# Kernel tuning notes

Hardware: AMD Instinct MI355X
Metric: run time of the kernel (lower is better)

## Reference

```python
import jax, jax.numpy as jnp
import numpy as np

RADIUS = 1.3
N_SAMPLES = 256
STEP = 0.0176


def trilinear(grid, pts):
    """grid: [C, D, H, W]; pts: [M, 3] in [-1, 1] ordered (x, y, z) like torch grid_sample
    (x indexes W, y indexes H, z indexes D), align_corners=True, border padding.
    Returns [M, C]."""
    C, D, H, W = grid.shape
    sizes = jnp.asarray([W, H, D], dtype=pts.dtype)
    co = jnp.clip((pts + 1.0) * 0.5 * (sizes - 1.0), 0.0, sizes - 1.0)
    c0 = jnp.floor(co)
    f = co - c0                                   # [M,3] trilinear weights
    i0 = c0.astype(jnp.int32)
    i1 = jnp.minimum(i0 + 1, jnp.asarray([W - 1, H - 1, D - 1], jnp.int32))
    gf = grid.reshape(C, -1)

    def gat(ix, iy, iz):                          # -> [M, C]
        return gf[:, (iz * H + iy) * W + ix].T

    x0, y0, z0 = i0[:, 0], i0[:, 1], i0[:, 2]
    x1, y1, z1 = i1[:, 0], i1[:, 1], i1[:, 2]
    wx, wy, wz = f[:, 0:1], f[:, 1:2], f[:, 2:3]
    out = (gat(x0, y0, z0) * (1 - wx) * (1 - wy) * (1 - wz)
         + gat(x1, y0, z0) * wx       * (1 - wy) * (1 - wz)
         + gat(x0, y1, z0) * (1 - wx) * wy       * (1 - wz)
         + gat(x1, y1, z0) * wx       * wy       * (1 - wz)
         + gat(x0, y0, z1) * (1 - wx) * (1 - wy) * wz
         + gat(x1, y0, z1) * wx       * (1 - wy) * wz
         + gat(x0, y1, z1) * (1 - wx) * wy       * wz
         + gat(x1, y1, z1) * wx       * wy       * wz)
    return out


def get_intersections(rays_o, dirn):
    """Ray / cube[-R,R]^3 intersection; N_SAMPLES uniform steps from entry point.
    Returns pts [B,N,3], t-values [B,N], validity mask [B,N]."""
    eps = 1e-9
    safe_d = jnp.where(jnp.abs(dirn) < eps, eps, dirn)
    inv = 1.0 / safe_d
    t1 = (-RADIUS - rays_o) * inv
    t2 = (RADIUS - rays_o) * inv
    tmin = jnp.max(jnp.minimum(t1, t2), axis=-1)
    tmax = jnp.min(jnp.maximum(t1, t2), axis=-1)
    tnear = jnp.maximum(tmin, 0.0)
    hit = tmax > tnear                                          # [B]
    t = tnear[:, None] + STEP * jnp.arange(N_SAMPLES, dtype=rays_o.dtype)[None, :]
    pts = rays_o[:, None, :] + t[..., None] * dirn[:, None, :]  # [B,N,3]
    mask = (t < tmax[:, None]) & hit[:, None]
    return pts, t, mask


def setup_inputs() -> dict:
    key = jax.random.key(0)
    ks = jax.random.split(key, 12)
    B, R, GD, FD, NF, HW = 2048, 128, 3, 32, 32, 64
    o = jax.random.normal(ks[0], (B, 3), dtype=jnp.float32)
    rays_o = o / jnp.linalg.norm(o, axis=-1, keepdims=True) * (2.0 * RADIUS)
    rays_d = -rays_o + 0.3 * jax.random.normal(ks[1], (B, 3), dtype=jnp.float32)
    G1 = 0.01 * jax.random.normal(ks[2], (GD, R, R, R), dtype=jnp.float32)
    F = 0.05 * jax.random.normal(ks[3], (FD, NF, NF, NF), dtype=jnp.float32)
    s = 0.1
    return {
        'rays_o': rays_o, 'rays_d': rays_d, 'G1': G1, 'F': F,
        'Wd1': s * jax.random.normal(ks[4], (FD, HW), dtype=jnp.float32),
        'bd1': jnp.zeros((HW,), jnp.float32),
        'Wd2': s * jax.random.normal(ks[5], (HW, 1), dtype=jnp.float32),
        'bd2': jnp.zeros((1,), jnp.float32),
        'Wc1': s * jax.random.normal(ks[6], (FD + 3, HW), dtype=jnp.float32),
        'bc1': jnp.zeros((HW,), jnp.float32),
        'Wc2': s * jax.random.normal(ks[7], (HW, 3), dtype=jnp.float32),
        'bc2': jnp.zeros((3,), jnp.float32),
    }


def reference(rays_o, rays_d, G1, F, Wd1, bd1, Wd2, bd2, Wc1, bc1, Wc2, bc2):
    B = rays_o.shape[0]
    dirn = rays_d / jnp.linalg.norm(rays_d, axis=-1, keepdims=True)
    pts, t, mask = get_intersections(rays_o, dirn)           # [B,N,3],[B,N],[B,N]
    pts_n = (pts / RADIUS).reshape(-1, 3)                     # [M,3] in ~[-1,1]

    # nested multi-grid trilinear lookups: coords -> G1 -> F
    g1v = trilinear(G1, pts_n)                                # [M,3]
    feats = trilinear(F, g1v)                                 # [M,feature_dim]

    # density MLP (1 hidden layer, width 64)
    h = jax.nn.relu(feats @ Wd1 + bd1)
    sigma = (h @ Wd2 + bd2)[:, 0].reshape(B, N_SAMPLES)
    sigma = jnp.where(mask, sigma, 0.0)

    # sigma -> alpha -> compositing weights (abs_light)
    dists = jnp.concatenate([t[:, 1:] - t[:, :-1],
                             jnp.full((B, 1), STEP, t.dtype)], axis=1)
    alpha = 1.0 - jnp.exp(-jax.nn.relu(sigma) * dists)
    T = jnp.cumprod(1.0 - alpha + 1e-10, axis=1)
    T_excl = jnp.concatenate([jnp.ones((B, 1), alpha.dtype), T[:, :-1]], axis=1)
    weights = alpha * T_excl                                  # [B,N]

    # color MLP conditioned on view direction
    dflat = jnp.broadcast_to(dirn[:, None, :], (B, N_SAMPLES, 3)).reshape(-1, 3)
    hc = jax.nn.relu(jnp.concatenate([feats, dflat], axis=-1) @ Wc1 + bc1)
    rgb = jax.nn.sigmoid((hc @ Wc2 + bc2).reshape(B, N_SAMPLES, 3))
    rgb = jnp.where(mask[..., None], rgb, 0.0)

    out = jnp.sum(weights[..., None] * rgb, axis=1)           # [B,3]
    acc = jnp.sum(weights, axis=1)
    return out + (1.0 - acc)[:, None]                         # white background
```

## Files before the change

### kernel.cpp

```cpp
#include <hip/hip_runtime.h>
#include <hip/hip_fp16.h>
#include <math.h>

#define NSAMP 256

typedef _Float16 f16;
typedef _Float16 f16x8 __attribute__((ext_vector_type(8)));
typedef float    f32x4 __attribute__((ext_vector_type(4)));

__global__ __launch_bounds__(256) void transpose_F(
    const float* __restrict__ Fg, float* __restrict__ Ft)
{
    const int j = blockIdx.x * 256 + threadIdx.x;
    float4 o[8];
    #pragma unroll
    for (int q = 0; q < 8; ++q) {
        o[q].x = Fg[(size_t)(4*q+0)*32768 + j];
        o[q].y = Fg[(size_t)(4*q+1)*32768 + j];
        o[q].z = Fg[(size_t)(4*q+2)*32768 + j];
        o[q].w = Fg[(size_t)(4*q+3)*32768 + j];
    }
    float4* dst = (float4*)(Ft + (size_t)j * 32);
    #pragma unroll
    for (int q = 0; q < 8; ++q) dst[q] = o[q];
}

__global__ __launch_bounds__(256) void pack_bfrags(
    const float* __restrict__ Wd1, const float* __restrict__ Wc1,
    f16* __restrict__ Bd, f16* __restrict__ Bc)
{
    const int idx  = threadIdx.x;
    const int nt   = idx >> 6;
    const int lane = idx & 63;
    const int j    = nt*16 + (lane & 15);
    const int k0   = (lane >> 4) * 8;
    f16x8 vd, vc;
    #pragma unroll
    for (int i = 0; i < 8; ++i) {
        vd[i] = (f16)Wd1[(k0+i)*64 + j];
        vc[i] = (f16)Wc1[(k0+i)*64 + j];
    }
    *(f16x8*)(Bd + ((size_t)(nt*64+lane))*8) = vd;
    *(f16x8*)(Bc + ((size_t)(nt*64+lane))*8) = vc;
}

template<bool USE_MFMA>
__global__ __launch_bounds__(256) __attribute__((amdgpu_waves_per_eu(2, 6)))
void nerf_fused(
    const float* __restrict__ rays_o, const float* __restrict__ rays_d,
    const float* __restrict__ G1, const float* __restrict__ Fg,
    const float* __restrict__ Wd1, const float* __restrict__ bd1,
    const float* __restrict__ Wd2, const float* __restrict__ bd2,
    const float* __restrict__ Wc1, const float* __restrict__ bc1,
    const float* __restrict__ Wc2, const float* __restrict__ bc2,
    const float* __restrict__ Ft,
    const f16* __restrict__ Bd, const f16* __restrict__ Bc,
    float* __restrict__ out)
{
    const float RADIUS = 1.3f;
    const float STEP = 0.0176f;

    const int b    = blockIdx.x;
    const int tid  = threadIdx.x;
    const int lane = tid & 63;
    const int wv   = tid >> 6;

    __shared__ __align__(16) f16 feats_lds[256][32];
    __shared__ float sig_lds[256];
    __shared__ f16   rgb_lds[256][4];
    __shared__ float s_wtot[4];
    __shared__ float s_red[4][4];

    const float ox = rays_o[b*3+0], oy = rays_o[b*3+1], oz = rays_o[b*3+2];
    const float rdx = rays_d[b*3+0], rdy = rays_d[b*3+1], rdz = rays_d[b*3+2];
    const float rn  = sqrtf(rdx*rdx + rdy*rdy + rdz*rdz);
    const float dxn = rdx/rn, dyn = rdy/rn, dzn = rdz/rn;

    float sd, inv, t1, t2, tmin, tmax;
    sd = (fabsf(dxn) < 1e-9f) ? 1e-9f : dxn; inv = 1.0f/sd;
    t1 = (-RADIUS - ox)*inv; t2 = (RADIUS - ox)*inv;
    tmin = fminf(t1,t2); tmax = fmaxf(t1,t2);
    sd = (fabsf(dyn) < 1e-9f) ? 1e-9f : dyn; inv = 1.0f/sd;
    t1 = (-RADIUS - oy)*inv; t2 = (RADIUS - oy)*inv;
    tmin = fmaxf(tmin, fminf(t1,t2)); tmax = fminf(tmax, fmaxf(t1,t2));
    sd = (fabsf(dzn) < 1e-9f) ? 1e-9f : dzn; inv = 1.0f/sd;
    t1 = (-RADIUS - oz)*inv; t2 = (RADIUS - oz)*inv;
    tmin = fmaxf(tmin, fminf(t1,t2)); tmax = fminf(tmax, fmaxf(t1,t2));

    const float tnear = fmaxf(tmin, 0.0f);
    const bool  hit   = tmax > tnear;
    const float t     = tnear + STEP * (float)tid;
    const bool  mask  = (t < tmax) && hit;

    const bool wave_active = __any(mask);

    float sigma = 0.0f, rr = 0.0f, rg = 0.0f, rb = 0.0f;

    float feats[32];
    if (wave_active) {
        const float invR = 1.0f / RADIUS;
        const float px = (ox + t*dxn) * invR;
        const float py = (oy + t*dyn) * invR;
        const float pz = (oz + t*dzn) * invR;

        float cox = fminf(fmaxf((px+1.0f)*0.5f*127.0f, 0.0f), 127.0f);
        float coy = fminf(fmaxf((py+1.0f)*0.5f*127.0f, 0.0f), 127.0f);
        float coz = fminf(fmaxf((pz+1.0f)*0.5f*127.0f, 0.0f), 127.0f);
        int x0 = (int)floorf(cox); float fx = cox - (float)x0; int x1 = min(x0+1, 127);
        int y0 = (int)floorf(coy); float fy = coy - (float)y0; int y1 = min(y0+1, 127);
        int z0 = (int)floorf(coz); float fz = coz - (float)z0; int z1 = min(z0+1, 127);

        {
            const float wx0 = 1.0f-fx, wx1 = fx;
            const float wy0 = 1.0f-fy, wy1 = fy;
            const float wz0 = 1.0f-fz, wz1 = fz;
            const float w000 = wx0*wy0*wz0, w100 = wx1*wy0*wz0;
            const float w010 = wx0*wy1*wz0, w110 = wx1*wy1*wz0;
            const float w001 = wx0*wy0*wz1, w101 = wx1*wy0*wz1;
            const float w011 = wx0*wy1*wz1, w111 = wx1*wy1*wz1;
            const int i000 = (z0*128 + y0)*128 + x0;
            const int dxo = x1 - x0;
            const int dyo = (y1 - y0)*128;
            const int dzo = (z1 - z0)*16384;
            const int i100 = i000 + dxo,       i010 = i000 + dyo;
            const int i110 = i000 + dyo + dxo, i001 = i000 + dzo;
            const int i101 = i000 + dzo + dxo, i011 = i000 + dzo + dyo;
            const int i111 = i000 + dzo + dyo + dxo;

            float g[3];
            #pragma unroll
            for (int c = 0; c < 3; ++c) {
                const float* gp = G1 + (size_t)c * 2097152;
                g[c] = w000*gp[i000] + w100*gp[i100] + w010*gp[i010] + w110*gp[i110]
                     + w001*gp[i001] + w101*gp[i101] + w011*gp[i011] + w111*gp[i111];
            }

            cox = fminf(fmaxf((g[0]+1.0f)*0.5f*31.0f, 0.0f), 31.0f);
            coy = fminf(fmaxf((g[1]+1.0f)*0.5f*31.0f, 0.0f), 31.0f);
            coz = fminf(fmaxf((g[2]+1.0f)*0.5f*31.0f, 0.0f), 31.0f);
            x0 = (int)floorf(cox); fx = cox - (float)x0; x1 = min(x0+1, 31);
            y0 = (int)floorf(coy); fy = coy - (float)y0; y1 = min(y0+1, 31);
            z0 = (int)floorf(coz); fz = coz - (float)z0; z1 = min(z0+1, 31);
        }

        #pragma unroll
        for (int c = 0; c < 32; ++c) feats[c] = 0.0f;
        {
            const float wx0 = 1.0f-fx, wx1 = fx;
            const float wy0 = 1.0f-fy, wy1 = fy;
            const float wz0 = 1.0f-fz, wz1 = fz;
            const int j000 = (z0*32 + y0)*32 + x0;
            const int dxo = x1 - x0;
            const int dyo = (y1 - y0)*32;
            const int dzo = (z1 - z0)*1024;

            const int   jidx[8] = { j000,           j000+dxo,
                                    j000+dyo,       j000+dyo+dxo,
                                    j000+dzo,       j000+dzo+dxo,
                                    j000+dzo+dyo,   j000+dzo+dyo+dxo };
            const float jwt[8]  = { wx0*wy0*wz0, wx1*wy0*wz0,
                                    wx0*wy1*wz0, wx1*wy1*wz0,
                                    wx0*wy0*wz1, wx1*wy0*wz1,
                                    wx0*wy1*wz1, wx1*wy1*wz1 };

            if (USE_MFMA) {
                #pragma unroll
                for (int corner = 0; corner < 8; ++corner) {
                    const float4* fp = (const float4*)(Ft + (size_t)jidx[corner] * 32);
                    const float w = jwt[corner];
                    #pragma unroll
                    for (int q = 0; q < 8; ++q) {
                        const float4 v = fp[q];
                        feats[4*q+0] += w * v.x;
                        feats[4*q+1] += w * v.y;
                        feats[4*q+2] += w * v.z;
                        feats[4*q+3] += w * v.w;
                    }
                }
            } else {
                #pragma unroll
                for (int corner = 0; corner < 8; ++corner) {
                    const float w = jwt[corner];
                    const int  j  = jidx[corner];
                    #pragma unroll
                    for (int c = 0; c < 32; ++c)
                        feats[c] += w * Fg[(size_t)c * 32768 + j];
                }
            }
        }
    }

    if (USE_MFMA) {
        if (wave_active) {
            #pragma unroll
            for (int gq = 0; gq < 4; ++gq) {
                f16x8 h;
                #pragma unroll
                for (int i = 0; i < 8; ++i) h[i] = (f16)feats[gq*8+i];
                *(f16x8*)&feats_lds[tid][gq*8] = h;
            }
        }
        __syncthreads();

        if (wave_active) {
            const int lane15 = lane & 15;
            const int laneg  = lane >> 4;

            float bias_d[4], bias_c[4], wd2v[4];
            float wc2r[4], wc2g[4], wc2b[4];
            #pragma unroll
            for (int nt = 0; nt < 4; ++nt) {
                const int j = nt*16 + lane15;
                bias_d[nt] = bd1[j];
                bias_c[nt] = bc1[j] + dxn*Wc1[32*64+j] + dyn*Wc1[33*64+j] + dzn*Wc1[34*64+j];
                wd2v[nt]   = Wd2[j];
                wc2r[nt]   = Wc2[j*3+0];
                wc2g[nt]   = Wc2[j*3+1];
                wc2b[nt]   = Wc2[j*3+2];
            }
            f16x8 bdf[4], bcf[4];
            #pragma unroll
            for (int nt = 0; nt < 4; ++nt) {
                bdf[nt] = *(const f16x8*)(Bd + ((size_t)(nt*64+lane))*8);
                bcf[nt] = *(const f16x8*)(Bc + ((size_t)(nt*64+lane))*8);
            }

            #pragma unroll
            for (int mt = 0; mt < 4; ++mt) {
                const int arow = wv*64 + mt*16 + lane15;
                const f16x8 af = *(const f16x8*)&feats_lds[arow][laneg*8];

                f32x4 accd[4], accc[4];
                #pragma unroll
                for (int nt = 0; nt < 4; ++nt) {
                    const float bdv = bias_d[nt], bcv = bias_c[nt];
                    accd[nt] = (f32x4){bdv, bdv, bdv, bdv};
                    accc[nt] = (f32x4){bcv, bcv, bcv, bcv};
                }
                #pragma unroll
                for (int nt = 0; nt < 4; ++nt) {
                    accd[nt] = __builtin_amdgcn_mfma_f32_16x16x32_f16(af, bdf[nt], accd[nt], 0, 0, 0);
                    accc[nt] = __builtin_amdgcn_mfma_f32_16x16x32_f16(af, bcf[nt], accc[nt], 0, 0, 0);
                }

                float ss[4] = {0.f,0.f,0.f,0.f};
                float sr[4] = {0.f,0.f,0.f,0.f};
                float sg[4] = {0.f,0.f,0.f,0.f};
                float sb[4] = {0.f,0.f,0.f,0.f};
                #pragma unroll
                for (int nt = 0; nt < 4; ++nt) {
                    #pragma unroll
                    for (int reg = 0; reg < 4; ++reg) {
                        const float hd = fmaxf(accd[nt][reg], 0.0f);
                        ss[reg] += hd * wd2v[nt];
                        const float hc = fmaxf(accc[nt][reg], 0.0f);
                        sr[reg] += hc * wc2r[nt];
                        sg[reg] += hc * wc2g[nt];
                        sb[reg] += hc * wc2b[nt];
                    }
                }
                #pragma unroll
                for (int st = 1; st < 16; st <<= 1) {
                    #pragma unroll
                    for (int reg = 0; reg < 4; ++reg) {
                        ss[reg] += __shfl_xor(ss[reg], st, 64);
                        sr[reg] += __shfl_xor(sr[reg], st, 64);
                        sg[reg] += __shfl_xor(sg[reg], st, 64);
                        sb[reg] += __shfl_xor(sb[reg], st, 64);
                    }
                }
                if (lane15 == 0) {
                    const int base = wv*64 + mt*16 + laneg*4;
                    #pragma unroll
                    for (int reg = 0; reg < 4; ++reg) {
                        sig_lds[base+reg]    = ss[reg];
                        rgb_lds[base+reg][0] = (f16)sr[reg];
                        rgb_lds[base+reg][1] = (f16)sg[reg];
                        rgb_lds[base+reg][2] = (f16)sb[reg];
                    }
                }
            }
        }
        __syncthreads();

        {
            const float sv  = sig_lds[tid];
            const float crv = (float)rgb_lds[tid][0] + bc2[0];
            const float cgv = (float)rgb_lds[tid][1] + bc2[1];
            const float cbv = (float)rgb_lds[tid][2] + bc2[2];
            sigma = mask ? (sv + bd2[0]) : 0.0f;
            rr = mask ? 1.0f/(1.0f + expf(-crv)) : 0.0f;
            rg = mask ? 1.0f/(1.0f + expf(-cgv)) : 0.0f;
            rb = mask ? 1.0f/(1.0f + expf(-cbv)) : 0.0f;
        }
    } else {
        if (wave_active) {
            float sg1 = bd2[0], cr = 0.0f, cg = 0.0f, cb = 0.0f;
            for (int j0 = 0; j0 < 64; j0 += 8) {
                float ad[8], ac[8];
                #pragma unroll
                for (int jj = 0; jj < 8; ++jj) {
                    ad[jj] = bd1[j0+jj];
                    ac[jj] = bc1[j0+jj] + dxn*Wc1[32*64 + j0 + jj]
                                        + dyn*Wc1[33*64 + j0 + jj]
                                        + dzn*Wc1[34*64 + j0 + jj];
                }
                #pragma unroll
                for (int k = 0; k < 32; ++k) {
                    const float fv = feats[k];
                    #pragma unroll
                    for (int jj = 0; jj < 8; ++jj) {
                        ad[jj] += fv * Wd1[k*64 + j0 + jj];
                        ac[jj] += fv * Wc1[k*64 + j0 + jj];
                    }
                }
                #pragma unroll
                for (int jj = 0; jj < 8; ++jj) {
                    sg1 += fmaxf(ad[jj], 0.0f) * Wd2[j0+jj];
                    const float hc = fmaxf(ac[jj], 0.0f);
                    cr += hc * Wc2[(j0+jj)*3 + 0];
                    cg += hc * Wc2[(j0+jj)*3 + 1];
                    cb += hc * Wc2[(j0+jj)*3 + 2];
                }
            }
            cr += bc2[0]; cg += bc2[1]; cb += bc2[2];
            sigma = mask ? sg1 : 0.0f;
            rr = mask ? 1.0f/(1.0f + expf(-cr)) : 0.0f;
            rg = mask ? 1.0f/(1.0f + expf(-cg)) : 0.0f;
            rb = mask ? 1.0f/(1.0f + expf(-cb)) : 0.0f;
        }
    }

    const float alpha = 1.0f - expf(-fmaxf(sigma, 0.0f) * STEP);
    float p = 1.0f - alpha + 1e-10f;

    float scan = p;
    #pragma unroll
    for (int off = 1; off < 64; off <<= 1) {
        const float n = __shfl_up(scan, off, 64);
        if (lane >= off) scan *= n;
    }
    if (lane == 63) s_wtot[wv] = scan;
    __syncthreads();

    float pre = 1.0f;
    #pragma unroll
    for (int q = 0; q < 4; ++q) if (q < wv) pre *= s_wtot[q];
    float excl = __shfl_up(scan, 1, 64);
    if (lane == 0) excl = 1.0f;
    const float Texcl = pre * excl;

    const float w = alpha * Texcl;
    float sw  = w;
    float swr = w * rr, swg = w * rg, swb = w * rb;

    #pragma unroll
    for (int off = 32; off > 0; off >>= 1) {
        sw  += __shfl_down(sw,  off, 64);
        swr += __shfl_down(swr, off, 64);
        swg += __shfl_down(swg, off, 64);
        swb += __shfl_down(swb, off, 64);
    }
    if (lane == 0) {
        s_red[wv][0] = sw;  s_red[wv][1] = swr;
        s_red[wv][2] = swg; s_red[wv][3] = swb;
    }
    __syncthreads();
    if (tid == 0) {
        float W = 0.0f, R = 0.0f, Gc = 0.0f, Bc2_ = 0.0f;
        #pragma unroll
        for (int q = 0; q < 4; ++q) {
            W  += s_red[q][0]; R  += s_red[q][1];
            Gc += s_red[q][2]; Bc2_ += s_red[q][3];
        }
        const float bg = 1.0f - W;
        out[b*3+0] = R  + bg;
        out[b*3+1] = Gc + bg;
        out[b*3+2] = Bc2_ + bg;
    }
}

extern "C" void kernel_launch(void* const* d_in, const int* in_sizes, int n_in,
                              void* d_out, int out_size, void* d_ws, size_t ws_size,
                              hipStream_t stream) {
    const float* rays_o = (const float*)d_in[0];
    const float* rays_d = (const float*)d_in[1];
    const float* G1     = (const float*)d_in[2];
    const float* Fg     = (const float*)d_in[3];
    const float* Wd1    = (const float*)d_in[4];
    const float* bd1    = (const float*)d_in[5];
    const float* Wd2    = (const float*)d_in[6];
    const float* bd2    = (const float*)d_in[7];
    const float* Wc1    = (const float*)d_in[8];
    const float* bc1    = (const float*)d_in[9];
    const float* Wc2    = (const float*)d_in[10];
    const float* bc2    = (const float*)d_in[11];
    float* out = (float*)d_out;

    const int B = in_sizes[0] / 3;
    const size_t ft_bytes = (size_t)32768 * 32 * sizeof(float);
    const size_t bf_bytes = (size_t)4 * 64 * 8 * sizeof(f16);

    if (ws_size >= ft_bytes + 2*bf_bytes) {
        float* Ft = (float*)d_ws;
        f16*   Bd = (f16*)((char*)d_ws + ft_bytes);
        f16*   Bc = (f16*)((char*)d_ws + ft_bytes + bf_bytes);
        transpose_F<<<dim3(128), dim3(256), 0, stream>>>(Fg, Ft);
        pack_bfrags<<<dim3(1), dim3(256), 0, stream>>>(Wd1, Wc1, Bd, Bc);
        nerf_fused<true><<<dim3(B), dim3(NSAMP), 0, stream>>>(
            rays_o, rays_d, G1, Fg, Wd1, bd1, Wd2, bd2, Wc1, bc1, Wc2, bc2,
            Ft, Bd, Bc, out);
    } else {
        nerf_fused<false><<<dim3(B), dim3(NSAMP), 0, stream>>>(
            rays_o, rays_d, G1, Fg, Wd1, bd1, Wd2, bd2, Wc1, bc1, Wc2, bc2,
            Fg, (const f16*)d_ws, (const f16*)d_ws, out);
    }
}
```

Before: 144.9 us.

## Repack grids to fp16 with x-neighbour pairing to halve trilinear gathers

Adds a per-call pre-pass that repacks the 128^3 coordinate grid G1 into fp16 records. Each 16-byte record holds a voxel's 3 channels plus those of its x+1 neighbour. The feature table is also transposed to fp16, with a zero padding row so adjacent rows serve as the x+1 corner. Each trilinear lookup then needs 4 wide loads instead of 8 per corner set, which is meant to cut scattered gather traffic and instruction count. In exchange, every call reads and writes tens of MB of repacked G1 data, and the first-level grid values lose precision in fp16, which feeds into the second-level coordinates.

```diff
diff --git a/kernel.cpp b/kernel.cpp
--- a/kernel.cpp
+++ b/kernel.cpp
@@ -5,24 +5,46 @@
 #define NSAMP 256
 
 typedef _Float16 f16;
+typedef _Float16 f16x4 __attribute__((ext_vector_type(4)));
 typedef _Float16 f16x8 __attribute__((ext_vector_type(8)));
 typedef float    f32x4 __attribute__((ext_vector_type(4)));
 
-__global__ __launch_bounds__(256) void transpose_F(
-    const float* __restrict__ Fg, float* __restrict__ Ft)
+__global__ __launch_bounds__(256) void transpose_F16(
+    const float* __restrict__ Fg, f16* __restrict__ Ft)
 {
     const int j = blockIdx.x * 256 + threadIdx.x;
-    float4 o[8];
-    #pragma unroll
-    for (int q = 0; q < 8; ++q) {
-        o[q].x = Fg[(size_t)(4*q+0)*32768 + j];
-        o[q].y = Fg[(size_t)(4*q+1)*32768 + j];
-        o[q].z = Fg[(size_t)(4*q+2)*32768 + j];
-        o[q].w = Fg[(size_t)(4*q+3)*32768 + j];
-    }
-    float4* dst = (float4*)(Ft + (size_t)j * 32);
-    #pragma unroll
-    for (int q = 0; q < 8; ++q) dst[q] = o[q];
+    f16x8 o[4];
+    #pragma unroll
+    for (int q = 0; q < 4; ++q)
+        #pragma unroll
+        for (int i = 0; i < 8; ++i)
+            o[q][i] = (f16)Fg[(size_t)(8*q+i)*32768 + j];
+    f16* dst = Ft + (size_t)j * 32;
+    #pragma unroll
+    for (int q = 0; q < 4; ++q) *(f16x8*)(dst + q*8) = o[q];
+    if (j == 32767) {
+        f16x8 z = {};
+        f16* pd = Ft + (size_t)32768 * 32;
+        #pragma unroll
+        for (int q = 0; q < 4; ++q) *(f16x8*)(pd + q*8) = z;
+    }
+}
+
+__global__ __launch_bounds__(256) void transpose_G1p(
+    const float* __restrict__ G1, f16x8* __restrict__ G1p)
+{
+    const int v  = blockIdx.x * 256 + threadIdx.x;
+    const int vn = min(v + 1, 2097151);
+    f16x8 o;
+    o[0] = (f16)G1[v];
+    o[1] = (f16)G1[2097152 + v];
+    o[2] = (f16)G1[2*2097152 + v];
+    o[3] = (f16)0.0f;
+    o[4] = (f16)G1[vn];
+    o[5] = (f16)G1[2097152 + vn];
+    o[6] = (f16)G1[2*2097152 + vn];
+    o[7] = (f16)0.0f;
+    G1p[v] = o;
 }
 
 __global__ __launch_bounds__(256) void pack_bfrags(
@@ -44,16 +66,14 @@
     *(f16x8*)(Bc + ((size_t)(nt*64+lane))*8) = vc;
 }
 
-template<bool USE_MFMA>
 __global__ __launch_bounds__(256) __attribute__((amdgpu_waves_per_eu(2, 6)))
-void nerf_fused(
+void nerf_fused_opt(
     const float* __restrict__ rays_o, const float* __restrict__ rays_d,
-    const float* __restrict__ G1, const float* __restrict__ Fg,
-    const float* __restrict__ Wd1, const float* __restrict__ bd1,
-    const float* __restrict__ Wd2, const float* __restrict__ bd2,
+    const f16x8* __restrict__ G1p, const f16* __restrict__ Ft16,
+    const float* __restrict__ bd1, const float* __restrict__ Wd2,
+    const float* __restrict__ bd2,
     const float* __restrict__ Wc1, const float* __restrict__ bc1,
     const float* __restrict__ Wc2, const float* __restrict__ bc2,
-    const float* __restrict__ Ft,
     const f16* __restrict__ Bd, const f16* __restrict__ Bc,
     float* __restrict__ out)
 {
@@ -65,7 +85,7 @@
     const int lane = tid & 63;
     const int wv   = tid >> 6;
 
-    __shared__ __align__(16) f16 feats_lds[256][32];
+    __shared__ __align__(16) f16 feats_lds[256][40];
     __shared__ float sig_lds[256];
     __shared__ f16   rgb_lds[256][4];
     __shared__ float s_wtot[4];
@@ -106,10 +126,283 @@
         float cox = fminf(fmaxf((px+1.0f)*0.5f*127.0f, 0.0f), 127.0f);
         float coy = fminf(fmaxf((py+1.0f)*0.5f*127.0f, 0.0f), 127.0f);
         float coz = fminf(fmaxf((pz+1.0f)*0.5f*127.0f, 0.0f), 127.0f);
+        int x0 = (int)floorf(cox); float fx = cox - (float)x0;
+        int y0 = (int)floorf(coy); float fy = coy - (float)y0; int y1 = min(y0+1, 127);
+        int z0 = (int)floorf(coz); float fz = coz - (float)z0; int z1 = min(z0+1, 127);
+
+        {
+            const float wx0 = 1.0f-fx, wx1 = fx;
+            const float wy0 = 1.0f-fy, wy1 = fy;
+            const float wz0 = 1.0f-fz, wz1 = fz;
+            const int i000 = (z0*128 + y0)*128 + x0;
+            const int dyo = (y1 - y0)*128;
+            const int dzo = (z1 - z0)*16384;
+
+            const f16x8 p00 = G1p[i000];
+            const f16x8 p10 = G1p[i000 + dyo];
+            const f16x8 p01 = G1p[i000 + dzo];
+            const f16x8 p11 = G1p[i000 + dyo + dzo];
+
+            const float a00 = wy0*wz0, a10 = wy1*wz0, a01 = wy0*wz1, a11 = wy1*wz1;
+
+            float g[3];
+            #pragma unroll
+            for (int c = 0; c < 3; ++c) {
+                g[c] = a00*(wx0*(float)p00[c] + wx1*(float)p00[4+c])
+                     + a10*(wx0*(float)p10[c] + wx1*(float)p10[4+c])
+                     + a01*(wx0*(float)p01[c] + wx1*(float)p01[4+c])
+                     + a11*(wx0*(float)p11[c] + wx1*(float)p11[4+c]);
+            }
+
+            cox = fminf(fmaxf((g[0]+1.0f)*0.5f*31.0f, 0.0f), 31.0f);
+            coy = fminf(fmaxf((g[1]+1.0f)*0.5f*31.0f, 0.0f), 31.0f);
+            coz = fminf(fmaxf((g[2]+1.0f)*0.5f*31.0f, 0.0f), 31.0f);
+            x0 = (int)floorf(cox); fx = cox - (float)x0;
+            y0 = (int)floorf(coy); fy = coy - (float)y0; y1 = min(y0+1, 31);
+            z0 = (int)floorf(coz); fz = coz - (float)z0; z1 = min(z0+1, 31);
+        }
+
+        #pragma unroll
+        for (int c = 0; c < 32; ++c) feats[c] = 0.0f;
+        {
+            const float wx0 = 1.0f-fx, wx1 = fx;
+            const float wy0 = 1.0f-fy, wy1 = fy;
+            const float wz0 = 1.0f-fz, wz1 = fz;
+            const int j000 = (z0*32 + y0)*32 + x0;
+            const int dyo = (y1 - y0)*32;
+            const int dzo = (z1 - z0)*1024;
+
+            const int   jp[4] = { j000, j000+dyo, j000+dzo, j000+dyo+dzo };
+            const float ap[4] = { wy0*wz0, wy1*wz0, wy0*wz1, wy1*wz1 };
+
+            #pragma unroll
+            for (int p = 0; p < 4; ++p) {
+                const f16* base = Ft16 + (size_t)jp[p] * 32;
+                const float aw = ap[p]*wx0, bw = ap[p]*wx1;
+                f16x8 lo[4], hi[4];
+                #pragma unroll
+                for (int q = 0; q < 4; ++q) lo[q] = *(const f16x8*)(base + q*8);
+                #pragma unroll
+                for (int q = 0; q < 4; ++q) hi[q] = *(const f16x8*)(base + 32 + q*8);
+                #pragma unroll
+                for (int q = 0; q < 4; ++q)
+                    #pragma unroll
+                    for (int i = 0; i < 8; ++i)
+                        feats[8*q+i] += aw*(float)lo[q][i] + bw*(float)hi[q][i];
+            }
+        }
+    }
+
+    if (wave_active) {
+        #pragma unroll
+        for (int gq = 0; gq < 4; ++gq) {
+            f16x8 h;
+            #pragma unroll
+            for (int i = 0; i < 8; ++i) h[i] = (f16)feats[gq*8+i];
+            *(f16x8*)&feats_lds[tid][gq*8] = h;
+        }
+    }
+    __syncthreads();
+
+    if (wave_active) {
+        const int lane15 = lane & 15;
+        const int laneg  = lane >> 4;
+
+        float bias_d[4], bias_c[4], wd2v[4];
+        float wc2r[4], wc2g[4], wc2b[4];
+        #pragma unroll
+        for (int nt = 0; nt < 4; ++nt) {
+            const int j = nt*16 + lane15;
+            bias_d[nt] = bd1[j];
+            bias_c[nt] = bc1[j] + dxn*Wc1[32*64+j] + dyn*Wc1[33*64+j] + dzn*Wc1[34*64+j];
+            wd2v[nt]   = Wd2[j];
+            wc2r[nt]   = Wc2[j*3+0];
+            wc2g[nt]   = Wc2[j*3+1];
+            wc2b[nt]   = Wc2[j*3+2];
+        }
+        f16x8 bdf[4], bcf[4];
+        #pragma unroll
+        for (int nt = 0; nt < 4; ++nt) {
+            bdf[nt] = *(const f16x8*)(Bd + ((size_t)(nt*64+lane))*8);
+            bcf[nt] = *(const f16x8*)(Bc + ((size_t)(nt*64+lane))*8);
+        }
+
+        #pragma unroll
+        for (int mt = 0; mt < 4; ++mt) {
+            const int arow = wv*64 + mt*16 + lane15;
+            const f16x8 af = *(const f16x8*)&feats_lds[arow][laneg*8];
+
+            f32x4 accd[4], accc[4];
+            #pragma unroll
+            for (int nt = 0; nt < 4; ++nt) {
+                const float bdv = bias_d[nt], bcv = bias_c[nt];
+                accd[nt] = (f32x4){bdv, bdv, bdv, bdv};
+                accc[nt] = (f32x4){bcv, bcv, bcv, bcv};
+            }
+            #pragma unroll
+            for (int nt = 0; nt < 4; ++nt) {
+                accd[nt] = __builtin_amdgcn_mfma_f32_16x16x32_f16(af, bdf[nt], accd[nt], 0, 0, 0);
+                accc[nt] = __builtin_amdgcn_mfma_f32_16x16x32_f16(af, bcf[nt], accc[nt], 0, 0, 0);
+            }
+
+            float ss[4] = {0.f,0.f,0.f,0.f};
+            float sr[4] = {0.f,0.f,0.f,0.f};
+            float sg[4] = {0.f,0.f,0.f,0.f};
+            float sb[4] = {0.f,0.f,0.f,0.f};
+            #pragma unroll
+            for (int nt = 0; nt < 4; ++nt) {
+                #pragma unroll
+                for (int reg = 0; reg < 4; ++reg) {
+                    const float hd = fmaxf(accd[nt][reg], 0.0f);
+                    ss[reg] += hd * wd2v[nt];
+                    const float hc = fmaxf(accc[nt][reg], 0.0f);
+                    sr[reg] += hc * wc2r[nt];
+                    sg[reg] += hc * wc2g[nt];
+                    sb[reg] += hc * wc2b[nt];
+                }
+            }
+            #pragma unroll
+            for (int st = 1; st < 16; st <<= 1) {
+                #pragma unroll
+                for (int reg = 0; reg < 4; ++reg) {
+                    ss[reg] += __shfl_xor(ss[reg], st, 64);
+                    sr[reg] += __shfl_xor(sr[reg], st, 64);
+                    sg[reg] += __shfl_xor(sg[reg], st, 64);
+                    sb[reg] += __shfl_xor(sb[reg], st, 64);
+                }
+            }
+            if (lane15 == 0) {
+                const int base = wv*64 + mt*16 + laneg*4;
+                #pragma unroll
+                for (int reg = 0; reg < 4; ++reg) {
+                    sig_lds[base+reg]    = ss[reg];
+                    rgb_lds[base+reg][0] = (f16)sr[reg];
+                    rgb_lds[base+reg][1] = (f16)sg[reg];
+                    rgb_lds[base+reg][2] = (f16)sb[reg];
+                }
+            }
+        }
+    }
+    __syncthreads();
+
+    {
+        const float sv  = sig_lds[tid];
+        const float crv = (float)rgb_lds[tid][0] + bc2[0];
+        const float cgv = (float)rgb_lds[tid][1] + bc2[1];
+        const float cbv = (float)rgb_lds[tid][2] + bc2[2];
+        sigma = mask ? (sv + bd2[0]) : 0.0f;
+        rr = mask ? 1.0f/(1.0f + expf(-crv)) : 0.0f;
+        rg = mask ? 1.0f/(1.0f + expf(-cgv)) : 0.0f;
+        rb = mask ? 1.0f/(1.0f + expf(-cbv)) : 0.0f;
+    }
+
+    const float alpha = 1.0f - expf(-fmaxf(sigma, 0.0f) * STEP);
+    float p = 1.0f - alpha + 1e-10f;
+
+    float scan = p;
+    #pragma unroll
+    for (int off = 1; off < 64; off <<= 1) {
+        const float n = __shfl_up(scan, off, 64);
+        if (lane >= off) scan *= n;
+    }
+    if (lane == 63) s_wtot[wv] = scan;
+    __syncthreads();
+
+    float pre = 1.0f;
+    #pragma unroll
+    for (int q = 0; q < 4; ++q) if (q < wv) pre *= s_wtot[q];
+    float excl = __shfl_up(scan, 1, 64);
+    if (lane == 0) excl = 1.0f;
+    const float Texcl = pre * excl;
+
+    const float w = alpha * Texcl;
+    float sw  = w;
+    float swr = w * rr, swg = w * rg, swb = w * rb;
+
+    #pragma unroll
+    for (int off = 32; off > 0; off >>= 1) {
+        sw  += __shfl_down(sw,  off, 64);
+        swr += __shfl_down(swr, off, 64);
+        swg += __shfl_down(swg, off, 64);
+        swb += __shfl_down(swb, off, 64);
+    }
+    if (lane == 0) {
+        s_red[wv][0] = sw;  s_red[wv][1] = swr;
+        s_red[wv][2] = swg; s_red[wv][3] = swb;
+    }
+    __syncthreads();
+    if (tid == 0) {
+        float W = 0.0f, R = 0.0f, Gc = 0.0f, Bc_ = 0.0f;
+        #pragma unroll
+        for (int q = 0; q < 4; ++q) {
+            W  += s_red[q][0]; R  += s_red[q][1];
+            Gc += s_red[q][2]; Bc_ += s_red[q][3];
+        }
+        const float bg = 1.0f - W;
+        out[b*3+0] = R   + bg;
+        out[b*3+1] = Gc  + bg;
+        out[b*3+2] = Bc_ + bg;
+    }
+}
+
+__global__ __launch_bounds__(256) __attribute__((amdgpu_waves_per_eu(2, 6)))
+void nerf_fused_naive(
+    const float* __restrict__ rays_o, const float* __restrict__ rays_d,
+    const float* __restrict__ G1, const float* __restrict__ Fg,
+    const float* __restrict__ Wd1, const float* __restrict__ bd1,
+    const float* __restrict__ Wd2, const float* __restrict__ bd2,
+    const float* __restrict__ Wc1, const float* __restrict__ bc1,
+    const float* __restrict__ Wc2, const float* __restrict__ bc2,
+    float* __restrict__ out)
+{
+    const float RADIUS = 1.3f;
+    const float STEP = 0.0176f;
+
+    const int b    = blockIdx.x;
+    const int tid  = threadIdx.x;
+    const int lane = tid & 63;
+    const int wv   = tid >> 6;
+
+    __shared__ float s_wtot[4];
+    __shared__ float s_red[4][4];
+
+    const float ox = rays_o[b*3+0], oy = rays_o[b*3+1], oz = rays_o[b*3+2];
+    const float rdx = rays_d[b*3+0], rdy = rays_d[b*3+1], rdz = rays_d[b*3+2];
+    const float rn  = sqrtf(rdx*rdx + rdy*rdy + rdz*rdz);
+    const float dxn = rdx/rn, dyn = rdy/rn, dzn = rdz/rn;
+
+    float sd, inv, t1, t2, tmin, tmax;
+    sd = (fabsf(dxn) < 1e-9f) ? 1e-9f : dxn; inv = 1.0f/sd;
+    t1 = (-RADIUS - ox)*inv; t2 = (RADIUS - ox)*inv;
+    tmin = fminf(t1,t2); tmax = fmaxf(t1,t2);
+    sd = (fabsf(dyn) < 1e-9f) ? 1e-9f : dyn; inv = 1.0f/sd;
+    t1 = (-RADIUS - oy)*inv; t2 = (RADIUS - oy)*inv;
+    tmin = fmaxf(tmin, fminf(t1,t2)); tmax = fminf(tmax, fmaxf(t1,t2));
+    sd = (fabsf(dzn) < 1e-9f) ? 1e-9f : dzn; inv = 1.0f/sd;
+    t1 = (-RADIUS - oz)*inv; t2 = (RADIUS - oz)*inv;
+    tmin = fmaxf(tmin, fminf(t1,t2)); tmax = fminf(tmax, fmaxf(t1,t2));
+
+    const float tnear = fmaxf(tmin, 0.0f);
+    const bool  hit   = tmax > tnear;
+    const float t     = tnear + STEP * (float)tid;
+    const bool  mask  = (t < tmax) && hit;
+
+    float sigma = 0.0f, rr = 0.0f, rg = 0.0f, rb = 0.0f;
+
+    if (__any(mask)) {
+        const float invR = 1.0f / RADIUS;
+        const float px = (ox + t*dxn) * invR;
+        const float py = (oy + t*dyn) * invR;
+        const float pz = (oz + t*dzn) * invR;
+
+        float cox = fminf(fmaxf((px+1.0f)*0.5f*127.0f, 0.0f), 127.0f);
+        float coy = fminf(fmaxf((py+1.0f)*0.5f*127.0f, 0.0f), 127.0f);
+        float coz = fminf(fmaxf((pz+1.0f)*0.5f*127.0f, 0.0f), 127.0f);
         int x0 = (int)floorf(cox); float fx = cox - (float)x0; int x1 = min(x0+1, 127);
         int y0 = (int)floorf(coy); float fy = coy - (float)y0; int y1 = min(y0+1, 127);
         int z0 = (int)floorf(coz); float fz = coz - (float)z0; int z1 = min(z0+1, 127);
 
+        float feats[32];
         {
             const float wx0 = 1.0f-fx, wx1 = fx;
             const float wy0 = 1.0f-fy, wy1 = fy;
@@ -141,194 +434,64 @@
             x0 = (int)floorf(cox); fx = cox - (float)x0; x1 = min(x0+1, 31);
             y0 = (int)floorf(coy); fy = coy - (float)y0; y1 = min(y0+1, 31);
             z0 = (int)floorf(coz); fz = coz - (float)z0; z1 = min(z0+1, 31);
-        }
-
-        #pragma unroll
-        for (int c = 0; c < 32; ++c) feats[c] = 0.0f;
-        {
-            const float wx0 = 1.0f-fx, wx1 = fx;
-            const float wy0 = 1.0f-fy, wy1 = fy;
-            const float wz0 = 1.0f-fz, wz1 = fz;
+
+            const float vx0 = 1.0f-fx, vx1 = fx;
+            const float vy0 = 1.0f-fy, vy1 = fy;
+            const float vz0 = 1.0f-fz, vz1 = fz;
+            const float u000 = vx0*vy0*vz0, u100 = vx1*vy0*vz0;
+            const float u010 = vx0*vy1*vz0, u110 = vx1*vy1*vz0;
+            const float u001 = vx0*vy0*vz1, u101 = vx1*vy0*vz1;
+            const float u011 = vx0*vy1*vz1, u111 = vx1*vy1*vz1;
             const int j000 = (z0*32 + y0)*32 + x0;
-            const int dxo = x1 - x0;
-            const int dyo = (y1 - y0)*32;
-            const int dzo = (z1 - z0)*1024;
-
-            const int   jidx[8] = { j000,           j000+dxo,
-                                    j000+dyo,       j000+dyo+dxo,
-                                    j000+dzo,       j000+dzo+dxo,
-                                    j000+dzo+dyo,   j000+dzo+dyo+dxo };
-            const float jwt[8]  = { wx0*wy0*wz0, wx1*wy0*wz0,
-                                    wx0*wy1*wz0, wx1*wy1*wz0,
-                                    wx0*wy0*wz1, wx1*wy0*wz1,
-                                    wx0*wy1*wz1, wx1*wy1*wz1 };
-
-            if (USE_MFMA) {
-                #pragma unroll
-                for (int corner = 0; corner < 8; ++corner) {
-                    const float4* fp = (const float4*)(Ft + (size_t)jidx[corner] * 32);
-                    const float w = jwt[corner];
-                    #pragma unroll
-                    for (int q = 0; q < 8; ++q) {
-                        const float4 v = fp[q];
-                        feats[4*q+0] += w * v.x;
-                        feats[4*q+1] += w * v.y;
-                        feats[4*q+2] += w * v.z;
-                        feats[4*q+3] += w * v.w;
-                    }
+            const int exo = x1 - x0;
+            const int eyo = (y1 - y0)*32;
+            const int ezo = (z1 - z0)*1024;
+            const int j100 = j000 + exo,       j010 = j000 + eyo;
+            const int j110 = j000 + eyo + exo, j001 = j000 + ezo;
+            const int j101 = j000 + ezo + exo, j011 = j000 + ezo + eyo;
+            const int j111 = j000 + ezo + eyo + exo;
+
+            #pragma unroll
+            for (int c = 0; c < 32; ++c) {
+                const float* fp = Fg + (size_t)c * 32768;
+                feats[c] = u000*fp[j000] + u100*fp[j100] + u010*fp[j010] + u110*fp[j110]
+                         + u001*fp[j001] + u101*fp[j101] + u011*fp[j011] + u111*fp[j111];
+            }
+        }
+
+        float sg1 = bd2[0], cr = 0.0f, cg = 0.0f, cb = 0.0f;
+        for (int j0 = 0; j0 < 64; j0 += 8) {
+            float ad[8], ac[8];
+            #pragma unroll
+            for (int jj = 0; jj < 8; ++jj) {
+                ad[jj] = bd1[j0+jj];
+                ac[jj] = bc1[j0+jj] + dxn*Wc1[32*64 + j0 + jj]
+                                    + dyn*Wc1[33*64 + j0 + jj]
+                                    + dzn*Wc1[34*64 + j0 + jj];
+            }
+            #pragma unroll
+            for (int k = 0; k < 32; ++k) {
+                const float fv = feats[k];
+                #pragma unroll
+                for (int jj = 0; jj < 8; ++jj) {
+                    ad[jj] += fv * Wd1[k*64 + j0 + jj];
+                    ac[jj] += fv * Wc1[k*64 + j0 + jj];
                 }
-            } else {
-                #pragma unroll
-                for (int corner = 0; corner < 8; ++corner) {
-                    const float w = jwt[corner];
-                    const int  j  = jidx[corner];
-                    #pragma unroll
-                    for (int c = 0; c < 32; ++c)
-                        feats[c] += w * Fg[(size_t)c * 32768 + j];
-                }
-            }
-        }
-    }
-
-    if (USE_MFMA) {
-        if (wave_active) {
-            #pragma unroll
-            for (int gq = 0; gq < 4; ++gq) {
-                f16x8 h;
-                #pragma unroll
-                for (int i = 0; i < 8; ++i) h[i] = (f16)feats[gq*8+i];
-                *(f16x8*)&feats_lds[tid][gq*8] = h;
-            }
-        }
-        __syncthreads();
-
-        if (wave_active) {
-            const int lane15 = lane & 15;
-            const int laneg  = lane >> 4;
-
-            float bias_d[4], bias_c[4], wd2v[4];
-            float wc2r[4], wc2g[4], wc2b[4];
-            #pragma unroll
-            for (int nt = 0; nt < 4; ++nt) {
-                const int j = nt*16 + lane15;
-                bias_d[nt] = bd1[j];
-                bias_c[nt] = bc1[j] + dxn*Wc1[32*64+j] + dyn*Wc1[33*64+j] + dzn*Wc1[34*64+j];
-                wd2v[nt]   = Wd2[j];
-                wc2r[nt]   = Wc2[j*3+0];
-                wc2g[nt]   = Wc2[j*3+1];
-                wc2b[nt]   = Wc2[j*3+2];
-            }
-            f16x8 bdf[4], bcf[4];
-            #pragma unroll
-            for (int nt = 0; nt < 4; ++nt) {
-                bdf[nt] = *(const f16x8*)(Bd + ((size_t)(nt*64+lane))*8);
-                bcf[nt] = *(const f16x8*)(Bc + ((size_t)(nt*64+lane))*8);
-            }
-
-            #pragma unroll
-            for (int mt = 0; mt < 4; ++mt) {
-                const int arow = wv*64 + mt*16 + lane15;
-                const f16x8 af = *(const f16x8*)&feats_lds[arow][laneg*8];
-
-                f32x4 accd[4], accc[4];
-                #pragma unroll
-                for (int nt = 0; nt < 4; ++nt) {
-                    const float bdv = bias_d[nt], bcv = bias_c[nt];
-                    accd[nt] = (f32x4){bdv, bdv, bdv, bdv};
-                    accc[nt] = (f32x4){bcv, bcv, bcv, bcv};
-                }
-                #pragma unroll
-                for (int nt = 0; nt < 4; ++nt) {
-                    accd[nt] = __builtin_amdgcn_mfma_f32_16x16x32_f16(af, bdf[nt], accd[nt], 0, 0, 0);
-                    accc[nt] = __builtin_amdgcn_mfma_f32_16x16x32_f16(af, bcf[nt], accc[nt], 0, 0, 0);
-                }
-
-                float ss[4] = {0.f,0.f,0.f,0.f};
-                float sr[4] = {0.f,0.f,0.f,0.f};
-                float sg[4] = {0.f,0.f,0.f,0.f};
-                float sb[4] = {0.f,0.f,0.f,0.f};
-                #pragma unroll
-                for (int nt = 0; nt < 4; ++nt) {
-                    #pragma unroll
-                    for (int reg = 0; reg < 4; ++reg) {
-                        const float hd = fmaxf(accd[nt][reg], 0.0f);
-                        ss[reg] += hd * wd2v[nt];
-                        const float hc = fmaxf(accc[nt][reg], 0.0f);
-                        sr[reg] += hc * wc2r[nt];
-                        sg[reg] += hc * wc2g[nt];
-                        sb[reg] += hc * wc2b[nt];
-                    }
-                }
-                #pragma unroll
-                for (int st = 1; st < 16; st <<= 1) {
-                    #pragma unroll
-                    for (int reg = 0; reg < 4; ++reg) {
-                        ss[reg] += __shfl_xor(ss[reg], st, 64);
-                        sr[reg] += __shfl_xor(sr[reg], st, 64);
-                        sg[reg] += __shfl_xor(sg[reg], st, 64);
-                        sb[reg] += __shfl_xor(sb[reg], st, 64);
-                    }
-                }
-                if (lane15 == 0) {
-                    const int base = wv*64 + mt*16 + laneg*4;
-                    #pragma unroll
-                    for (int reg = 0; reg < 4; ++reg) {
-                        sig_lds[base+reg]    = ss[reg];
-                        rgb_lds[base+reg][0] = (f16)sr[reg];
-                        rgb_lds[base+reg][1] = (f16)sg[reg];
-                        rgb_lds[base+reg][2] = (f16)sb[reg];
-                    }
-                }
-            }
-        }
-        __syncthreads();
-
-        {
-            const float sv  = sig_lds[tid];
-            const float crv = (float)rgb_lds[tid][0] + bc2[0];
-            const float cgv = (float)rgb_lds[tid][1] + bc2[1];
-            const float cbv = (float)rgb_lds[tid][2] + bc2[2];
-            sigma = mask ? (sv + bd2[0]) : 0.0f;
-            rr = mask ? 1.0f/(1.0f + expf(-crv)) : 0.0f;
-            rg = mask ? 1.0f/(1.0f + expf(-cgv)) : 0.0f;
-            rb = mask ? 1.0f/(1.0f + expf(-cbv)) : 0.0f;
-        }
-    } else {
-        if (wave_active) {
-            float sg1 = bd2[0], cr = 0.0f, cg = 0.0f, cb = 0.0f;
-            for (int j0 = 0; j0 < 64; j0 += 8) {
-                float ad[8], ac[8];
-                #pragma unroll
-                for (int jj = 0; jj < 8; ++jj) {
-                    ad[jj] = bd1[j0+jj];
-                    ac[jj] = bc1[j0+jj] + dxn*Wc1[32*64 + j0 + jj]
-                                        + dyn*Wc1[33*64 + j0 + jj]
-                                        + dzn*Wc1[34*64 + j0 + jj];
-                }
-                #pragma unroll
-                for (int k = 0; k < 32; ++k) {
-                    const float fv = feats[k];
-                    #pragma unroll
-                    for (int jj = 0; jj < 8; ++jj) {
-                        ad[jj] += fv * Wd1[k*64 + j0 + jj];
-                        ac[jj] += fv * Wc1[k*64 + j0 + jj];
-                    }
-                }
-                #pragma unroll
-                for (int jj = 0; jj < 8; ++jj) {
-                    sg1 += fmaxf(ad[jj], 0.0f) * Wd2[j0+jj];
-                    const float hc = fmaxf(ac[jj], 0.0f);
-                    cr += hc * Wc2[(j0+jj)*3 + 0];
-                    cg += hc * Wc2[(j0+jj)*3 + 1];
-                    cb += hc * Wc2[(j0+jj)*3 + 2];
-                }
-            }
-            cr += bc2[0]; cg += bc2[1]; cb += bc2[2];
-            sigma = mask ? sg1 : 0.0f;
-            rr = mask ? 1.0f/(1.0f + expf(-cr)) : 0.0f;
-            rg = mask ? 1.0f/(1.0f + expf(-cg)) : 0.0f;
-            rb = mask ? 1.0f/(1.0f + expf(-cb)) : 0.0f;
-        }
+            }
+            #pragma unroll
+            for (int jj = 0; jj < 8; ++jj) {
+                sg1 += fmaxf(ad[jj], 0.0f) * Wd2[j0+jj];
+                const float hc = fmaxf(ac[jj], 0.0f);
+                cr += hc * Wc2[(j0+jj)*3 + 0];
+                cg += hc * Wc2[(j0+jj)*3 + 1];
+                cb += hc * Wc2[(j0+jj)*3 + 2];
+            }
+        }
+        cr += bc2[0]; cg += bc2[1]; cb += bc2[2];
+        sigma = mask ? sg1 : 0.0f;
+        rr = mask ? 1.0f/(1.0f + expf(-cr)) : 0.0f;
+        rg = mask ? 1.0f/(1.0f + expf(-cg)) : 0.0f;
+        rb = mask ? 1.0f/(1.0f + expf(-cb)) : 0.0f;
     }
 
     const float alpha = 1.0f - expf(-fmaxf(sigma, 0.0f) * STEP);
@@ -367,16 +530,16 @@
     }
     __syncthreads();
     if (tid == 0) {
-        float W = 0.0f, R = 0.0f, Gc = 0.0f, Bc2_ = 0.0f;
+        float W = 0.0f, R = 0.0f, Gc = 0.0f, Bc_ = 0.0f;
         #pragma unroll
         for (int q = 0; q < 4; ++q) {
             W  += s_red[q][0]; R  += s_red[q][1];
-            Gc += s_red[q][2]; Bc2_ += s_red[q][3];
+            Gc += s_red[q][2]; Bc_ += s_red[q][3];
         }
         const float bg = 1.0f - W;
-        out[b*3+0] = R  + bg;
-        out[b*3+1] = Gc + bg;
-        out[b*3+2] = Bc2_ + bg;
+        out[b*3+0] = R   + bg;
+        out[b*3+1] = Gc  + bg;
+        out[b*3+2] = Bc_ + bg;
     }
 }
 
@@ -398,21 +561,23 @@
     float* out = (float*)d_out;
 
     const int B = in_sizes[0] / 3;
-    const size_t ft_bytes = (size_t)32768 * 32 * sizeof(float);
-    const size_t bf_bytes = (size_t)4 * 64 * 8 * sizeof(f16);
-
-    if (ws_size >= ft_bytes + 2*bf_bytes) {
-        float* Ft = (float*)d_ws;
-        f16*   Bd = (f16*)((char*)d_ws + ft_bytes);
-        f16*   Bc = (f16*)((char*)d_ws + ft_bytes + bf_bytes);
-        transpose_F<<<dim3(128), dim3(256), 0, stream>>>(Fg, Ft);
+    const size_t ft16_bytes = (size_t)32769 * 32 * sizeof(f16);
+    const size_t g1p_bytes  = (size_t)2097152 * sizeof(f16x8);
+    const size_t bf_bytes   = (size_t)4 * 64 * 8 * sizeof(f16);
+
+    if (ws_size >= ft16_bytes + g1p_bytes + 2*bf_bytes) {
+        f16*   Ft16 = (f16*)d_ws;
+        f16x8* G1p  = (f16x8*)((char*)d_ws + ft16_bytes);
+        f16*   Bd   = (f16*)((char*)d_ws + ft16_bytes + g1p_bytes);
+        f16*   Bc   = (f16*)((char*)d_ws + ft16_bytes + g1p_bytes + bf_bytes);
+        transpose_F16<<<dim3(128), dim3(256), 0, stream>>>(Fg, Ft16);
+        transpose_G1p<<<dim3(8192), dim3(256), 0, stream>>>(G1, G1p);
         pack_bfrags<<<dim3(1), dim3(256), 0, stream>>>(Wd1, Wc1, Bd, Bc);
-        nerf_fused<true><<<dim3(B), dim3(NSAMP), 0, stream>>>(
-            rays_o, rays_d, G1, Fg, Wd1, bd1, Wd2, bd2, Wc1, bc1, Wc2, bc2,
-            Ft, Bd, Bc, out);
+        nerf_fused_opt<<<dim3(B), dim3(NSAMP), 0, stream>>>(
+            rays_o, rays_d, G1p, Ft16, bd1, Wd2, bd2, Wc1, bc1, Wc2, bc2,
+            Bd, Bc, out);
     } else {
-        nerf_fused<false><<<dim3(B), dim3(NSAMP), 0, stream>>>(
-            rays_o, rays_d, G1, Fg, Wd1, bd1, Wd2, bd2, Wc1, bc1, Wc2, bc2,
-            Fg, (const f16*)d_ws, (const f16*)d_ws, out);
+        nerf_fused_naive<<<dim3(B), dim3(NSAMP), 0, stream>>>(
+            rays_o, rays_d, G1, Fg, Wd1, bd1, Wd2, bd2, Wc1, bc1, Wc2, bc2, out);
     }
 }
```

New measurement: 142.0 us. -2.0%, faster.
